# Optimization experiments

Hardware: AMD Instinct MI355X
Metric: run time of the kernel (lower is better)

Reference implementation:

```python
import jax, jax.numpy as jnp
import numpy as np

DIM = 1024
HEADS = 16
HEAD_DIM = DIM // HEADS  # 64


def get_rope_matrix(seq_len: int, dim: int) -> jnp.ndarray:
    # rope[s, d] = concat(cos(s * inv_freq), sin(s * inv_freq))  -> (seq_len, dim)
    half = dim // 2
    inv_freq = 1.0 / (10000.0 ** (jnp.arange(half, dtype=jnp.float32) / half))
    sinusoid = jnp.arange(seq_len, dtype=jnp.float32)[:, None] * inv_freq[None, :]
    return jnp.concatenate([jnp.cos(sinusoid), jnp.sin(sinusoid)], axis=-1)


def setup_inputs() -> dict:
    key = jax.random.key(0)
    ks = jax.random.split(key, 6)
    B, T, D = 2, 2048, DIM
    scale = 1.0 / np.sqrt(D)
    return {
        "x": jax.random.normal(ks[0], (B, T, D), dtype=jnp.float32),
        "Wq": jax.random.normal(ks[1], (D, D), dtype=jnp.float32) * scale,
        "Wk": jax.random.normal(ks[2], (D, D), dtype=jnp.float32) * scale,
        "Wv": jax.random.normal(ks[3], (D, D), dtype=jnp.float32) * scale,
        "Wo": jax.random.normal(ks[4], (D, D), dtype=jnp.float32) * scale,
        "bo": jax.random.normal(ks[5], (D,), dtype=jnp.float32) * 0.01,
    }


def reference(x, Wq, Wk, Wv, Wo, bo):
    B, T, D = x.shape
    H, hd = HEADS, HEAD_DIM

    # projections -> (B, H, T, hd)
    def split_heads(y):
        return y.reshape(B, T, H, hd).transpose(0, 2, 1, 3)

    q = split_heads(x @ Wq)
    k = split_heads(x @ Wk)
    v = split_heads(x @ Wv)

    rope = get_rope_matrix(T, hd)  # (T, hd)

    # apply_rope(v, rope): einsum('...nd,sd->...ns') contracts head_dim -> (B,H,T,T)
    v_r = jnp.einsum('bhnd,sd->bhns', v, rope)

    scores = jax.nn.softmax(jnp.einsum('bhnd,bhmd->bhnm', q, k) / jnp.sqrt(jnp.float32(hd)), axis=-1)
    out = jnp.einsum('bhnm,bhms->bhns', scores, v_r)  # (B,H,T,T)

    # apply_rope(out, rope.T): out2[...,n,s] = sum_t out[...,n,t] * rope[t,s] -> (B,H,T,hd)
    out = jnp.einsum('bhnt,ts->bhns', out, rope)

    out = out.transpose(0, 2, 1, 3).reshape(B, T, D)
    return out @ Wo + bo
```

## Files before the change

kernel.cpp:

```cpp
#include <hip/hip_runtime.h>
#include <math.h>

#define DIM 1024
#define NH 16
#define HD 64
#define TT 2048
#define NTOK 4096

typedef __bf16 bf8v __attribute__((ext_vector_type(8)));
typedef float f4v __attribute__((ext_vector_type(4)));
typedef float f16v __attribute__((ext_vector_type(16)));
typedef unsigned short us8 __attribute__((ext_vector_type(8)));
typedef unsigned short us4 __attribute__((ext_vector_type(4)));
typedef unsigned int u4v __attribute__((ext_vector_type(4)));

static __device__ __forceinline__ unsigned short f2bf(float f) {
    unsigned int u = __float_as_uint(f);
    u += 0x7FFFu + ((u >> 16) & 1u);
    return (unsigned short)(u >> 16);
}
static __device__ __forceinline__ bf8v ld8(const unsigned short* p) {
    return __builtin_bit_cast(bf8v, *(const us8*)p);
}
static __device__ __forceinline__ void gl_lds(const unsigned short* g, unsigned short* l) {
    __builtin_amdgcn_global_load_lds((const __attribute__((address_space(1))) unsigned int*)(g),
                                     (__attribute__((address_space(3))) unsigned int*)(l), 16, 0, 0);
}

__global__ void k_prep(const float* __restrict__ x, unsigned short* __restrict__ xb,
                       const float* __restrict__ Wq, const float* __restrict__ Wk,
                       const float* __restrict__ Wv, unsigned short* __restrict__ wt,
                       float* __restrict__ rope, float* __restrict__ Rm) {
    int tid = threadIdx.x;
    int bb = blockIdx.x;
    if (bb < 4096) {
        int i = bb * 256 + tid;
        float4 v = ((const float4*)x)[i];
        us4 o;
        o[0] = f2bf(v.x); o[1] = f2bf(v.y); o[2] = f2bf(v.z); o[3] = f2bf(v.w);
        *(us4*)&xb[i * 4] = o;
    } else if (bb < 7168) {
        __shared__ float tile[32][33];
        bb -= 4096;
        int z = bb >> 10, rem = bb & 1023;
        int bx = rem & 31, by = rem >> 5;
        const float* W = (z == 0) ? Wq : ((z == 1) ? Wk : Wv);
        int tx = tid & 31, ty = tid >> 5;
        int c0 = bx * 32, k0 = by * 32;
#pragma unroll
        for (int j = 0; j < 4; j++)
            tile[ty + j * 8][tx] = W[(k0 + ty + j * 8) * DIM + c0 + tx];
        __syncthreads();
        unsigned short* out = wt + z * DIM * DIM;
#pragma unroll
        for (int j = 0; j < 4; j++)
            out[(c0 + ty + j * 8) * DIM + k0 + tx] = f2bf(tile[tx][ty + j * 8]);
    } else if (bb < 7680) {
        int i = (bb - 7168) * 256 + tid;
        int s = i >> 6, d = i & 63;
        float inv = exp2f(-(float)(d & 31) * (13.287712379549449f / 32.0f));
        float a = (float)s * inv;
        rope[i] = (d < 32) ? cosf(a) : sinf(a);
    } else {
        Rm[(bb - 7680) * 256 + tid] = 0.f;
    }
}

__global__ void k_R(const float* __restrict__ rope, float* __restrict__ R) {
    __shared__ float red[256];
    int d = blockIdx.x & 63, sg = blockIdx.x >> 6;
    int e = threadIdx.x & 63, sl = threadIdx.x >> 6;
    const float* rp = rope + (sg * 256 + sl * 64) * 64;
    float acc = 0.f;
    for (int s = 0; s < 64; s++)
        acc += rp[s * 64 + d] * rp[s * 64 + e];
    red[threadIdx.x] = acc;
    __syncthreads();
    if (sl == 0)
        atomicAdd(&R[d * 64 + e], (red[e] + red[e + 64]) + (red[e + 128] + red[e + 192]));
}

__global__ void k_wo2(const float* __restrict__ Wo, const float* __restrict__ R,
                      unsigned short* __restrict__ wo2t) {
    __shared__ float Ws[64 * 65];
    __shared__ float Rt[64 * 65];
    int tid = threadIdx.x;
    int h = blockIdx.y, j0 = blockIdx.x * 64;
    for (int idx = tid; idx < 4096; idx += 256) {
        int e = idx >> 6, j = idx & 63;
        Ws[e * 65 + j] = Wo[(h * 64 + e) * DIM + j0 + j];
        Rt[e * 65 + j] = R[j * 64 + e];
    }
    __syncthreads();
    int d = tid & 63, jb = (tid >> 6) * 16;
    float acc[16] = {};
    for (int e = 0; e < 64; e++) {
        float r = Rt[e * 65 + d];
#pragma unroll
        for (int jj = 0; jj < 16; jj++)
            acc[jj] += r * Ws[e * 65 + jb + jj];
    }
#pragma unroll
    for (int jj = 0; jj < 16; jj++)
        wo2t[(j0 + jb + jj) * DIM + h * 64 + d] = f2bf(acc[jj]);
}


__global__ __launch_bounds__(256, 3) void k_gemm_qkv(const unsigned short* __restrict__ A,
                                                     const unsigned short* __restrict__ Bt,
                                                     unsigned short* __restrict__ qk,
                                                     unsigned short* __restrict__ vt) {
    __shared__ unsigned short As[128 * 32];
    __shared__ unsigned short Bs[128 * 32];
    const int K = 1024;
    int tid = threadIdx.x;
    int lane = tid & 63, w = tid >> 6;
    int quad = lane >> 4, l16 = lane & 15;
    int m0 = blockIdx.y * 128, n0 = blockIdx.x * 128;
    int wm = (w >> 1) * 64, wn = (w & 1) * 64;

    int s0 = tid, s1 = 256 + tid;
    int r0 = s0 >> 2, cc0 = ((s0 & 3) ^ (r0 & 3)) * 8;
    int r1 = s1 >> 2, cc1 = ((s1 & 3) ^ (r1 & 3)) * 8;
    const unsigned short* Ag0 = A + (m0 + r0) * K + cc0;
    const unsigned short* Ag1 = A + (m0 + r1) * K + cc1;
    const unsigned short* Bg0 = Bt + (n0 + r0) * K + cc0;
    const unsigned short* Bg1 = Bt + (n0 + r1) * K + cc1;
    int qx = quad ^ (l16 & 3);

    f4v acc[4][4] = {};
    for (int k0 = 0; k0 < K; k0 += 32) {
        __syncthreads();
        gl_lds(Ag0 + k0, &As[s0 * 8]);
        gl_lds(Ag1 + k0, &As[s1 * 8]);
        gl_lds(Bg0 + k0, &Bs[s0 * 8]);
        gl_lds(Bg1 + k0, &Bs[s1 * 8]);
        __syncthreads();
        bf8v af[4], bf[4];
#pragma unroll
        for (int mt = 0; mt < 4; mt++)
            af[mt] = ld8(&As[(wm + mt * 16 + l16) * 32 + qx * 8]);
#pragma unroll
        for (int nt = 0; nt < 4; nt++)
            bf[nt] = ld8(&Bs[(wn + nt * 16 + l16) * 32 + qx * 8]);
#pragma unroll
        for (int mt = 0; mt < 4; mt++)
#pragma unroll
            for (int nt = 0; nt < 4; nt++)
                acc[mt][nt] = __builtin_amdgcn_mfma_f32_16x16x32_bf16(af[mt], bf[nt], acc[mt][nt], 0, 0, 0);
    }
#pragma unroll
    for (int mt = 0; mt < 4; mt++) {
#pragma unroll
        for (int nt = 0; nt < 4; nt++) {
            int gc = n0 + wn + nt * 16 + l16;
            int h = (gc >> 6) & 15;
            int d = gc & 63;
            if (gc < 2048) {
                float qs = (gc < 1024) ? 0.18033688011111793f : 1.0f;
                int mtx = gc >> 10;
                unsigned short* base = qk + mtx * (NTOK * DIM);
#pragma unroll
                for (int r = 0; r < 4; r++) {
                    int gm = m0 + wm + mt * 16 + quad * 4 + r;
                    int b = gm >> 11, t = gm & 2047;
                    base[((b * NH + h) * TT + t) * HD + d] = f2bf(acc[mt][nt][r] * qs);
                }
            } else {
                int gm0 = m0 + wm + mt * 16 + quad * 4;
                int b = gm0 >> 11, t = gm0 & 2047;
                us4 ov;
#pragma unroll
                for (int r = 0; r < 4; r++)
                    ov[r] = f2bf(acc[mt][nt][r]);
                *(us4*)&vt[(((b * NH + h) * HD) + d) * TT + t] = ov;
            }
        }
    }
}

__global__ __launch_bounds__(256, 2) void k_gemm_out(const unsigned short* __restrict__ Op,
                                                     const float* __restrict__ Ls,
                                                     const unsigned short* __restrict__ Bt,
                                                     const float* __restrict__ bo,
                                                     float* __restrict__ out) {
    __shared__ unsigned short As[64 * 32];
    __shared__ unsigned short Bs[128 * 32];
    const int K = 1024;
    int tid = threadIdx.x;
    int lane = tid & 63, w = tid >> 6;
    int quad = lane >> 4, l16 = lane & 15;
    int bid = blockIdx.x;
    int xcd = bid & 7, slot = bid >> 3;
    int y = xcd * 8 + (slot & 7);
    int x = slot >> 3;
    int m0 = y * 64, n0 = x * 128;
    int wn = w * 32;

    int rr = tid >> 2, cc = ((tid & 3) ^ (rr & 3)) * 8;
    int gm0 = m0 + rr;
    const unsigned short* Ag0 = Op + gm0 * K + cc;
    const unsigned short* Bg0 = Bt + (n0 + rr) * K + cc;
    const unsigned short* Bg1 = Bt + (n0 + 64 + rr) * K + cc;
    const float* L0 = Ls + (gm0 >> 11) * 16 * 2048 + (gm0 & 2047);
    int qx = quad ^ (l16 & 3);

    us8 pa0 = *(const us8*)(Ag0);
    us8 pc0 = *(const us8*)(Ag0 + NTOK * DIM);
    float pl00 = L0[0], pl01 = L0[65536];

    f4v acc[4][2] = {};
    for (int k0 = 0; k0 < K; k0 += 32) {
        __syncthreads();
        gl_lds(Bg0 + k0, &Bs[tid * 8]);
        gl_lds(Bg1 + k0, &Bs[(256 + tid) * 8]);
        {
            float inv0 = __builtin_amdgcn_rcpf(pl00 + pl01);
            u4v o0;
#pragma unroll
            for (int p = 0; p < 4; p++) {
                float va = (__uint_as_float((unsigned int)pa0[2 * p] << 16) +
                            __uint_as_float((unsigned int)pc0[2 * p] << 16)) * inv0;
                float vb = (__uint_as_float((unsigned int)pa0[2 * p + 1] << 16) +
                            __uint_as_float((unsigned int)pc0[2 * p + 1] << 16)) * inv0;
                unsigned int wd;
                asm("v_cvt_pk_bf16_f32 %0, %1, %2" : "=v"(wd) : "v"(va), "v"(vb));
                o0[p] = wd;
            }
            *(u4v*)&As[tid * 8] = o0;
        }
        __syncthreads();
        {
            int kn = (k0 + 32) & 1023;
            int hn = (kn + cc) >> 6;
            pa0 = *(const us8*)(Ag0 + kn);
            pc0 = *(const us8*)(Ag0 + NTOK * DIM + kn);
            pl00 = L0[hn * 2048]; pl01 = L0[65536 + hn * 2048];
        }
        bf8v af[4], bf[2];
#pragma unroll
        for (int mt = 0; mt < 4; mt++)
            af[mt] = ld8(&As[(mt * 16 + l16) * 32 + qx * 8]);
#pragma unroll
        for (int nt = 0; nt < 2; nt++)
            bf[nt] = ld8(&Bs[(wn + nt * 16 + l16) * 32 + qx * 8]);
#pragma unroll
        for (int mt = 0; mt < 4; mt++)
#pragma unroll
            for (int nt = 0; nt < 2; nt++)
                acc[mt][nt] = __builtin_amdgcn_mfma_f32_16x16x32_bf16(af[mt], bf[nt], acc[mt][nt], 0, 0, 0);
    }
#pragma unroll
    for (int mt = 0; mt < 4; mt++) {
#pragma unroll
        for (int nt = 0; nt < 2; nt++) {
            int gc = n0 + wn + nt * 16 + l16;
            float bias = bo[gc];
#pragma unroll
            for (int r = 0; r < 4; r++) {
                int gm = m0 + mt * 16 + quad * 4 + r;
                out[gm * DIM + gc] = acc[mt][nt][r] + bias;
            }
        }
    }
}

__global__ __launch_bounds__(256, 4) void k_flash(const unsigned short* __restrict__ qk,
                                                  const unsigned short* __restrict__ vt,
                                                  unsigned short* __restrict__ Op,
                                                  float* __restrict__ Ls) {
    __shared__ unsigned short Ks[2][64 * 64];
    __shared__ unsigned short Vs[2][64 * 64];
    int tid = threadIdx.x;
    int lane = tid & 63, w = tid >> 6;
    int q31 = lane & 31, hi = lane >> 5;
    int bid = blockIdx.x;
    int xcd = bid & 7, sl = bid >> 3;
    int bh = xcd * 4 + (sl & 3);
    int qt = (sl >> 2) & 15;
    int sp = sl >> 6;

    const unsigned short* Qg = qk + bh * (TT * HD);
    const unsigned short* Kg = qk + NTOK * DIM + bh * (TT * HD) + sp * 1024 * HD;
    const unsigned short* Vg = vt + bh * (HD * TT) + sp * 1024;

    int qrow = qt * 128 + w * 32 + q31;
    bf8v qf[4];
#pragma unroll
    for (int ks = 0; ks < 4; ks++)
        qf[ks] = ld8(Qg + qrow * HD + ks * 16 + hi * 8);

    int r0 = tid >> 3, sw = (tid & 7) ^ (r0 & 7);
    int offK0 = r0 * HD + sw * 8, offK1 = offK0 + 32 * HD;
    int offV0 = r0 * TT + sw * 8, offV1 = offV0 + 32 * TT;
    int dst0 = tid * 8, dst1 = dst0 + 2048;

#define STAGE(tile, bufsel) do {                                  \
        const unsigned short* kb_ = Kg + (tile) * 64 * HD;        \
        const unsigned short* vb_ = Vg + (tile) * 64;             \
        gl_lds(kb_ + offK0, &Ks[bufsel][dst0]);                   \
        gl_lds(kb_ + offK1, &Ks[bufsel][dst1]);                   \
        gl_lds(vb_ + offV0, &Vs[bufsel][dst0]);                   \
        gl_lds(vb_ + offV1, &Vs[bufsel][dst1]);                   \
    } while (0)

    STAGE(0, 0);
    STAGE(1, 1);

    f16v oacc[2] = {};
    float lsg = 0.f;
    int xsw = q31 & 7;

    for (int it = 0; it < 16; it++) {
        int cur = it & 1;
        if (it == 15) { asm volatile("s_waitcnt vmcnt(0)" ::: "memory"); }
        else          { asm volatile("s_waitcnt vmcnt(4)" ::: "memory"); }
        __builtin_amdgcn_s_barrier();
        asm volatile("" ::: "memory");

        const unsigned short* Kb = Ks[cur];
        const unsigned short* Vb = Vs[cur];

        bf8v kf0[4], kf1[4];
#pragma unroll
        for (int ks = 0; ks < 4; ks++) {
            kf0[ks] = ld8(&Kb[(q31) * 64 + ((2 * ks + hi) ^ xsw) * 8]);
            kf1[ks] = ld8(&Kb[(32 + q31) * 64 + ((2 * ks + hi) ^ xsw) * 8]);
        }
        f16v s0 = {}, s1 = {};
#pragma unroll
        for (int ks = 0; ks < 4; ks++) {
            s0 = __builtin_amdgcn_mfma_f32_32x32x16_bf16(kf0[ks], qf[ks], s0, 0, 0, 0);
            s1 = __builtin_amdgcn_mfma_f32_32x32x16_bf16(kf1[ks], qf[ks], s1, 0, 0, 0);
        }

        bf8v vf[2][4];
#pragma unroll
        for (int kk = 0; kk < 4; kk++) {
            vf[0][kk] = ld8(&Vb[(q31) * 64 + ((2 * kk + hi) ^ xsw) * 8]);
            vf[1][kk] = ld8(&Vb[(32 + q31) * 64 + ((2 * kk + hi) ^ xsw) * 8]);
        }

#pragma unroll
        for (int mt = 0; mt < 2; mt++) {
#pragma unroll
            for (int sub = 0; sub < 2; sub++) {
                const f16v& s = mt ? s1 : s0;
                float pe[8];
#pragma unroll
                for (int j = 0; j < 8; j++)
                    pe[j] = __builtin_amdgcn_exp2f(s[sub * 8 + j]);
                float t01 = pe[0] + pe[1], t23 = pe[2] + pe[3];
                float t45 = pe[4] + pe[5], t67 = pe[6] + pe[7];
                lsg += (t01 + t23) + (t45 + t67);
                unsigned int e0, e1, e2, e3;
                asm("v_cvt_pk_bf16_f32 %0, %1, %2" : "=v"(e0) : "v"(pe[0]), "v"(pe[1]));
                asm("v_cvt_pk_bf16_f32 %0, %1, %2" : "=v"(e1) : "v"(pe[2]), "v"(pe[3]));
                asm("v_cvt_pk_bf16_f32 %0, %1, %2" : "=v"(e2) : "v"(pe[4]), "v"(pe[5]));
                asm("v_cvt_pk_bf16_f32 %0, %1, %2" : "=v"(e3) : "v"(pe[6]), "v"(pe[7]));
                asm("v_permlane32_swap_b32 %0, %1" : "+v"(e0), "+v"(e2));
                asm("v_permlane32_swap_b32 %0, %1" : "+v"(e1), "+v"(e3));
                u4v pv = {e0, e1, e2, e3};
                bf8v pb = __builtin_bit_cast(bf8v, pv);
                int kk = mt * 2 + sub;
                oacc[0] = __builtin_amdgcn_mfma_f32_32x32x16_bf16(vf[0][kk], pb, oacc[0], 0, 0, 0);
                oacc[1] = __builtin_amdgcn_mfma_f32_32x32x16_bf16(vf[1][kk], pb, oacc[1], 0, 0, 0);
            }
        }

        __builtin_amdgcn_s_barrier();
        asm volatile("" ::: "memory");
        if (it < 14) STAGE(it + 2, cur);
    }
#undef STAGE

    float lsum = lsg + __shfl_xor(lsg, 32, 64);
    int b = bh >> 4, h = bh & 15;
    unsigned short* dst = Op + sp * (NTOK * DIM) + ((b * TT) + qrow) * DIM + h * HD + hi * 4;
#pragma unroll
    for (int mtd = 0; mtd < 2; mtd++) {
#pragma unroll
        for (int g4 = 0; g4 < 4; g4++) {
            us4 ov;
#pragma unroll
            for (int r = 0; r < 4; r++)
                ov[r] = f2bf(oacc[mtd][g4 * 4 + r]);
            *(us4*)&dst[mtd * 32 + g4 * 8] = ov;
        }
    }
    if (hi == 0)
        Ls[sp * 65536 + bh * 2048 + qrow] = lsum;
}

extern "C" void kernel_launch(void* const* d_in, const int* in_sizes, int n_in,
                              void* d_out, int out_size, void* d_ws, size_t ws_size,
                              hipStream_t stream) {
    const float* x  = (const float*)d_in[0];
    const float* Wq = (const float*)d_in[1];
    const float* Wk = (const float*)d_in[2];
    const float* Wv = (const float*)d_in[3];
    const float* Wo = (const float*)d_in[4];
    const float* bo = (const float*)d_in[5];
    float* out = (float*)d_out;
    char* ws = (char*)d_ws;

    unsigned short* Xb    = (unsigned short*)(ws);
    unsigned short* Wqkvt = (unsigned short*)(ws + 8388608);
    unsigned short* Op    = (unsigned short*)(ws);
    unsigned short* QK    = (unsigned short*)(ws + 16777216);
    unsigned short* Vt    = (unsigned short*)(ws + 33554432);
    unsigned short* Wo2t  = (unsigned short*)(ws + 50331648);
    float*          rope  = (float*)(ws + 52428800);
    float*          Rm    = (float*)(ws + 52953088);
    float*          Ls    = (float*)(ws + 52969472);

    hipLaunchKernelGGL(k_prep,     dim3(7696),   dim3(256), 0, stream, x, Xb, Wq, Wk, Wv, Wqkvt, rope, Rm);
    hipLaunchKernelGGL(k_R,        dim3(512),    dim3(256), 0, stream, rope, Rm);
    hipLaunchKernelGGL(k_wo2,      dim3(16, 16), dim3(256), 0, stream, Wo, Rm, Wo2t);
    hipLaunchKernelGGL(k_gemm_qkv, dim3(24, 32), dim3(256), 0, stream, Xb, Wqkvt, QK, Vt);
    hipLaunchKernelGGL(k_flash,    dim3(1024),   dim3(256), 0, stream, QK, Vt, Op, Ls);
    hipLaunchKernelGGL(k_gemm_out, dim3(512),    dim3(256), 0, stream, Op, Ls, Wo2t, bo, out);
}
```

Before: 202.8 us.

## Drop split-KV in flash attention and normalize in-kernel, simplify output GEMM

Removes the two-way split of the key sequence in the flash kernel. Each block now walks all 32 key tiles and divides by the row sum before storing bf16 output. The output GEMM can then load A directly into LDS with async copies, instead of merging two partials and rescaling per tile. This cuts partial-buffer traffic and combine work, but halves the flash grid to 512 blocks, lowers launch-bounds occupancy to 2, and lengthens the serial loop per block.

After: 190.2 us. -6.2%, faster.

```diff
diff --git a/kernel.cpp b/kernel.cpp
--- a/kernel.cpp
+++ b/kernel.cpp
@@ -179,8 +179,7 @@
     }
 }
 
-__global__ __launch_bounds__(256, 2) void k_gemm_out(const unsigned short* __restrict__ Op,
-                                                     const float* __restrict__ Ls,
+__global__ __launch_bounds__(256, 2) void k_gemm_out(const unsigned short* __restrict__ A,
                                                      const unsigned short* __restrict__ Bt,
                                                      const float* __restrict__ bo,
                                                      float* __restrict__ out) {
@@ -198,45 +197,18 @@
     int wn = w * 32;
 
     int rr = tid >> 2, cc = ((tid & 3) ^ (rr & 3)) * 8;
-    int gm0 = m0 + rr;
-    const unsigned short* Ag0 = Op + gm0 * K + cc;
+    const unsigned short* Ag0 = A + (m0 + rr) * K + cc;
     const unsigned short* Bg0 = Bt + (n0 + rr) * K + cc;
     const unsigned short* Bg1 = Bt + (n0 + 64 + rr) * K + cc;
-    const float* L0 = Ls + (gm0 >> 11) * 16 * 2048 + (gm0 & 2047);
     int qx = quad ^ (l16 & 3);
-
-    us8 pa0 = *(const us8*)(Ag0);
-    us8 pc0 = *(const us8*)(Ag0 + NTOK * DIM);
-    float pl00 = L0[0], pl01 = L0[65536];
 
     f4v acc[4][2] = {};
     for (int k0 = 0; k0 < K; k0 += 32) {
         __syncthreads();
+        gl_lds(Ag0 + k0, &As[tid * 8]);
         gl_lds(Bg0 + k0, &Bs[tid * 8]);
         gl_lds(Bg1 + k0, &Bs[(256 + tid) * 8]);
-        {
-            float inv0 = __builtin_amdgcn_rcpf(pl00 + pl01);
-            u4v o0;
-#pragma unroll
-            for (int p = 0; p < 4; p++) {
-                float va = (__uint_as_float((unsigned int)pa0[2 * p] << 16) +
-                            __uint_as_float((unsigned int)pc0[2 * p] << 16)) * inv0;
-                float vb = (__uint_as_float((unsigned int)pa0[2 * p + 1] << 16) +
-                            __uint_as_float((unsigned int)pc0[2 * p + 1] << 16)) * inv0;
-                unsigned int wd;
-                asm("v_cvt_pk_bf16_f32 %0, %1, %2" : "=v"(wd) : "v"(va), "v"(vb));
-                o0[p] = wd;
-            }
-            *(u4v*)&As[tid * 8] = o0;
-        }
-        __syncthreads();
-        {
-            int kn = (k0 + 32) & 1023;
-            int hn = (kn + cc) >> 6;
-            pa0 = *(const us8*)(Ag0 + kn);
-            pc0 = *(const us8*)(Ag0 + NTOK * DIM + kn);
-            pl00 = L0[hn * 2048]; pl01 = L0[65536 + hn * 2048];
-        }
+        __syncthreads();
         bf8v af[4], bf[2];
 #pragma unroll
         for (int mt = 0; mt < 4; mt++)
@@ -265,10 +237,9 @@
     }
 }
 
-__global__ __launch_bounds__(256, 4) void k_flash(const unsigned short* __restrict__ qk,
+__global__ __launch_bounds__(256, 2) void k_flash(const unsigned short* __restrict__ qk,
                                                   const unsigned short* __restrict__ vt,
-                                                  unsigned short* __restrict__ Op,
-                                                  float* __restrict__ Ls) {
+                                                  unsigned short* __restrict__ attn) {
     __shared__ unsigned short Ks[2][64 * 64];
     __shared__ unsigned short Vs[2][64 * 64];
     int tid = threadIdx.x;
@@ -277,12 +248,11 @@
     int bid = blockIdx.x;
     int xcd = bid & 7, sl = bid >> 3;
     int bh = xcd * 4 + (sl & 3);
-    int qt = (sl >> 2) & 15;
-    int sp = sl >> 6;
+    int qt = sl >> 2;
 
     const unsigned short* Qg = qk + bh * (TT * HD);
-    const unsigned short* Kg = qk + NTOK * DIM + bh * (TT * HD) + sp * 1024 * HD;
-    const unsigned short* Vg = vt + bh * (HD * TT) + sp * 1024;
+    const unsigned short* Kg = qk + NTOK * DIM + bh * (TT * HD);
+    const unsigned short* Vg = vt + bh * (HD * TT);
 
     int qrow = qt * 128 + w * 32 + q31;
     bf8v qf[4];
@@ -311,9 +281,9 @@
     float lsg = 0.f;
     int xsw = q31 & 7;
 
-    for (int it = 0; it < 16; it++) {
+    for (int it = 0; it < 32; it++) {
         int cur = it & 1;
-        if (it == 15) { asm volatile("s_waitcnt vmcnt(0)" ::: "memory"); }
+        if (it == 31) { asm volatile("s_waitcnt vmcnt(0)" ::: "memory"); }
         else          { asm volatile("s_waitcnt vmcnt(4)" ::: "memory"); }
         __builtin_amdgcn_s_barrier();
         asm volatile("" ::: "memory");
@@ -370,13 +340,14 @@
 
         __builtin_amdgcn_s_barrier();
         asm volatile("" ::: "memory");
-        if (it < 14) STAGE(it + 2, cur);
+        if (it < 30) STAGE(it + 2, cur);
     }
 #undef STAGE
 
     float lsum = lsg + __shfl_xor(lsg, 32, 64);
+    float inv = __builtin_amdgcn_rcpf(lsum);
     int b = bh >> 4, h = bh & 15;
-    unsigned short* dst = Op + sp * (NTOK * DIM) + ((b * TT) + qrow) * DIM + h * HD + hi * 4;
+    unsigned short* dst = attn + ((b * TT) + qrow) * DIM + h * HD + hi * 4;
 #pragma unroll
     for (int mtd = 0; mtd < 2; mtd++) {
 #pragma unroll
@@ -384,12 +355,10 @@
             us4 ov;
 #pragma unroll
             for (int r = 0; r < 4; r++)
-                ov[r] = f2bf(oacc[mtd][g4 * 4 + r]);
+                ov[r] = f2bf(oacc[mtd][g4 * 4 + r] * inv);
             *(us4*)&dst[mtd * 32 + g4 * 8] = ov;
         }
     }
-    if (hi == 0)
-        Ls[sp * 65536 + bh * 2048 + qrow] = lsum;
 }
 
 extern "C" void kernel_launch(void* const* d_in, const int* in_sizes, int n_in,
@@ -406,18 +375,17 @@
 
     unsigned short* Xb    = (unsigned short*)(ws);
     unsigned short* Wqkvt = (unsigned short*)(ws + 8388608);
-    unsigned short* Op    = (unsigned short*)(ws);
+    unsigned short* attn  = (unsigned short*)(ws);
     unsigned short* QK    = (unsigned short*)(ws + 16777216);
     unsigned short* Vt    = (unsigned short*)(ws + 33554432);
     unsigned short* Wo2t  = (unsigned short*)(ws + 50331648);
     float*          rope  = (float*)(ws + 52428800);
     float*          Rm    = (float*)(ws + 52953088);
-    float*          Ls    = (float*)(ws + 52969472);
 
     hipLaunchKernelGGL(k_prep,     dim3(7696),   dim3(256), 0, stream, x, Xb, Wq, Wk, Wv, Wqkvt, rope, Rm);
     hipLaunchKernelGGL(k_R,        dim3(512),    dim3(256), 0, stream, rope, Rm);
     hipLaunchKernelGGL(k_wo2,      dim3(16, 16), dim3(256), 0, stream, Wo, Rm, Wo2t);
     hipLaunchKernelGGL(k_gemm_qkv, dim3(24, 32), dim3(256), 0, stream, Xb, Wqkvt, QK, Vt);
-    hipLaunchKernelGGL(k_flash,    dim3(1024),   dim3(256), 0, stream, QK, Vt, Op, Ls);
-    hipLaunchKernelGGL(k_gemm_out, dim3(512),    dim3(256), 0, stream, Op, Ls, Wo2t, bo, out);
-}
+    hipLaunchKernelGGL(k_flash,    dim3(512),    dim3(256), 0, stream, QK, Vt, attn);
+    hipLaunchKernelGGL(k_gemm_out, dim3(512),    dim3(256), 0, stream, attn, Wo2t, bo, out);
+}
```
